# Optimization experiments

Hardware: AMD Instinct MI355X
Metric: run time of the kernel (lower is better)

## Reference

```python
import jax, jax.numpy as jnp
import numpy as np

N_FFT = 256
HOP = 64            # fft_stride
WIN_LEN = 1024      # window_length (samples)
STRIDE = 256        # MPF window stride (samples)
FS = 2000.0
BANDS = [(0.0, 25.0), (25.0, 50.0), (50.0, 100.0), (100.0, 200.0), (200.0, 400.0), (400.0, 1000.0)]


def setup_inputs() -> dict:
    key = jax.random.key(0)
    x = jax.random.normal(key, (8, 32, 16000), dtype=jnp.float32)
    return {"inputs": x}


def _mpf_forward(inputs):
    # --- channelwise STFT (center=False, onesided, hann periodic=False) ---
    window = jnp.asarray(np.hanning(N_FFT), dtype=inputs.dtype)  # matches torch.hann_window(periodic=False)
    wnorm = jnp.linalg.norm(window)
    B, C, T = inputs.shape
    n_frames = 1 + (T - N_FFT) // HOP
    fidx = np.arange(n_frames)[:, None] * HOP + np.arange(N_FFT)[None, :]
    frames = inputs[..., fidx]                       # (B, C, n_frames, n_fft)
    spec = jnp.fft.rfft(frames * window, axis=-1) / wnorm  # (B, C, n_frames, F)
    spec = jnp.swapaxes(spec, -1, -2)                # (B, C, F, n_frames)

    # --- sliding window over STFT frames ---
    size = WIN_LEN // HOP   # 16
    step = STRIDE // HOP    # 4
    n_win = (n_frames - size) // step + 1
    widx = np.arange(n_win)[:, None] * step + np.arange(size)[None, :]
    win = spec[..., widx]                            # (B, C, F, n_win, size)
    x = jnp.transpose(win, (0, 3, 2, 1, 4))          # (B, n_win, F, C, size)

    # --- cross-spectral density: X X^H / size, then |.|^2 ---
    csd = jnp.einsum('btfcw,btfdw->btfcd', x, jnp.conj(x)) / size
    csd = csd.real ** 2 + csd.imag ** 2              # (B, n_win, F, C, C) real

    # --- average FFT bins into frequency bands ---
    freqs = np.fft.rfftfreq(N_FFT, d=1.0 / FS)
    masks_np = np.stack([(freqs > lo) & (freqs <= hi) for lo, hi in BANDS]).astype(np.float32)
    masks = jnp.asarray(masks_np, dtype=csd.dtype)   # (n_bands, F)
    banded = jnp.einsum('btfcd,kf->btkcd', csd, masks) / masks.sum(axis=1)[None, None, :, None, None]

    # --- SPD matrix log via eigh, eigvals floored at 100*eps ---
    eigvals, eigvecs = jnp.linalg.eigh(banded)
    floor = 100.0 * jnp.finfo(banded.dtype).eps
    log_vals = jnp.log(jnp.maximum(eigvals, floor))
    out = jnp.einsum('...ij,...j,...kj->...ik', eigvecs, log_vals, eigvecs)

    # (batch, time, bands, c1, c2) -> (batch, bands, c1, c2, time)
    return jnp.transpose(out, (0, 2, 3, 4, 1))


def reference(inputs) -> jnp.ndarray:
    return _mpf_forward(inputs)
```

## Files before the change

kernel.cpp:

```cpp
#include <hip/hip_runtime.h>
#include <cstddef>

#define NFRM 247
#define NBIN 128
#define NC   32
#define NWIN 58
#define NMAT (8 * NWIN * 6)

__global__ __launch_bounds__(128) void k_stft(const float* __restrict__ x,
                                              float2* __restrict__ spec) {
  const int gid = blockIdx.x;
  const int fr  = gid % NFRM;
  const int bc  = gid / NFRM;
  const int tid = threadIdx.x;

  __shared__ float  xw[256];
  __shared__ float2 tw[256];
  __shared__ float2 Y[256];

  const float* xp = x + ((size_t)bc * 16000 + (size_t)fr * 64);

  #pragma unroll
  for (int k = 0; k < 2; ++k) {
    const int t = tid + k * 128;
    const float wv = 0.5f - 0.5f * __cosf((float)t * 0.024639942f);
    xw[t] = xp[t] * wv * 0.10226200f;
    float sv, cv;
    __sincosf((float)t * 0.024543693f, &sv, &cv);
    tw[t] = make_float2(cv, -sv);
  }
  __syncthreads();

  #pragma unroll
  for (int k = 0; k < 2; ++k) {
    const int e = tid + k * 128;
    const int f0 = e >> 4, t0 = e & 15;
    const int step = (f0 << 4) & 255;
    float re = 0.f, im = 0.f;
    int m = 0;
    #pragma unroll
    for (int t1 = 0; t1 < 16; ++t1) {
      const float v = xw[(t1 << 4) + t0];
      const float2 w = tw[m];
      re = fmaf(v, w.x, re);
      im = fmaf(v, w.y, im);
      m = (m + step) & 255;
    }
    Y[e] = make_float2(re, im);
  }
  __syncthreads();

  const int f = tid + 1;
  const int f0 = f & 15;
  float re = 0.f, im = 0.f;
  int m = 0;
  #pragma unroll
  for (int t0 = 0; t0 < 16; ++t0) {
    const float2 yv = Y[(f0 << 4) + t0];
    const float2 w = tw[m];
    re += yv.x * w.x - yv.y * w.y;
    im += yv.x * w.y + yv.y * w.x;
    m = (m + f) & 255;
  }
  const int b = bc >> 5, c = bc & 31;
  spec[(((size_t)b * NFRM + fr) * NBIN + (f - 1)) * NC + c] = make_float2(re, im);
}

__global__ __launch_bounds__(256) void k_csd(const float2* __restrict__ spec,
                                             float* __restrict__ part, int P) {
  const int bt  = blockIdx.x;
  const int p   = blockIdx.y;
  const int b   = bt / NWIN, t = bt % NWIN;
  const int tid = threadIdx.x;
  const int wv  = tid >> 6;
  const int lane = tid & 63;
  const int i0 = (lane >> 3) * 4;
  const int j0 = (lane & 7) * 4;

  __shared__ __align__(16) char smemraw[32768];
  float2 (*rng)[2][512] = reinterpret_cast<float2 (*)[2][512]>(smemraw);
  float* red = reinterpret_cast<float*>(smemraw);

  float bacc[6][16];
  #pragma unroll
  for (int k = 0; k < 6; ++k)
    #pragma unroll
    for (int e = 0; e < 16; ++e) bacc[k][e] = 0.f;

  const float2* sb = spec + (size_t)b * NFRM * NBIN * NC;
  const int itn = 32 / P;

  #define STG_LOAD(itl, dst)                                                     \
    {                                                                            \
      const int f_ = 1 + wv + 4 * (itn * p + (itl));                             \
      const float2* fp_ = sb + (size_t)(f_ - 1) * NC;                            \
      _Pragma("unroll")                                                          \
      for (int r = 0; r < 8; ++r) {                                              \
        const int e_ = lane + r * 64;                                            \
        dst[r] = fp_[(size_t)(t * 4 + (e_ >> 5)) * (NBIN * NC) + (e_ & 31)];     \
      }                                                                          \
    }

  {
    float2 stg[8];
    STG_LOAD(0, stg)
    float2* Xs = rng[wv][0];
    #pragma unroll
    for (int r = 0; r < 8; ++r) Xs[lane + r * 64] = stg[r];
  }

  for (int itl = 0; itl < itn; ++itl) {
    float2 stg2[8];
    if (itl + 1 < itn) STG_LOAD(itl + 1, stg2)

    const int f = 1 + wv + 4 * (itn * p + itl);
    const float2* Xs = rng[wv][itl & 1];

    float accRe[16], accIm[16];
    #pragma unroll
    for (int e = 0; e < 16; ++e) { accRe[e] = 0.f; accIm[e] = 0.f; }

    #pragma unroll
    for (int s = 0; s < 16; ++s) {
      float2 xi[4], xj[4];
      #pragma unroll
      for (int a = 0; a < 4; ++a) {
        xi[a] = Xs[s * 32 + i0 + a];
        xj[a] = Xs[s * 32 + j0 + a];
      }
      #pragma unroll
      for (int a = 0; a < 4; ++a)
        #pragma unroll
        for (int d = 0; d < 4; ++d) {
          const int e = a * 4 + d;
          accRe[e] = fmaf(xi[a].x, xj[d].x, fmaf(xi[a].y, xj[d].y, accRe[e]));
          accIm[e] = fmaf(xi[a].y, xj[d].x, fmaf(-xi[a].x, xj[d].y, accIm[e]));
        }
    }

    #define ACCB(K) { _Pragma("unroll") \
      for (int e = 0; e < 16; ++e) { float rr = accRe[e], ii = accIm[e]; \
        bacc[K][e] = fmaf(rr, rr, fmaf(ii, ii, bacc[K][e])); } }
    if      (f <= 3)  ACCB(0)
    else if (f <= 6)  ACCB(1)
    else if (f <= 12) ACCB(2)
    else if (f <= 25) ACCB(3)
    else if (f <= 51) ACCB(4)
    else              ACCB(5)
    #undef ACCB

    if (itl + 1 < itn) {
      float2* Xn = rng[wv][(itl + 1) & 1];
      #pragma unroll
      for (int r = 0; r < 8; ++r) Xn[lane + r * 64] = stg2[r];
    }
  }
  #undef STG_LOAD

  __syncthreads();

  for (int w2 = 0; w2 < 4; ++w2) {
    if (wv == w2) {
      #pragma unroll
      for (int k = 0; k < 6; ++k)
        #pragma unroll
        for (int a = 0; a < 4; ++a)
          #pragma unroll
          for (int d = 0; d < 4; ++d) {
            const int idx = k * 1024 + (i0 + a) * 32 + (j0 + d);
            const float v = bacc[k][a * 4 + d];
            if (w2 == 0) red[idx] = v; else red[idx] += v;
          }
    }
    __syncthreads();
  }

  float* op = part + ((size_t)p * (8 * NWIN) + bt) * 6144;
  for (int u = tid; u < 6144; u += 256) {
    const int k = u >> 10;
    float scl;
    if      (k <= 1) scl = 1.f / 768.f;
    else if (k == 2) scl = 1.f / 1536.f;
    else if (k == 3) scl = 1.f / 3328.f;
    else if (k == 4) scl = 1.f / 6656.f;
    else             scl = 1.f / 19712.f;
    op[u] = red[u] * scl;
  }
}

__global__ __launch_bounds__(64) void k_eig(const float* __restrict__ part,
                                            float* __restrict__ eigTmp, int P) {
  const int blk  = blockIdx.x;
  const int lane = threadIdx.x;
  const int h    = lane >> 5;
  const int c    = lane & 31;

  __shared__ float sA[32][36];
  __shared__ float sSc[32];

  for (int u = lane; u < 1024; u += 64) {
    const size_t base = (size_t)blk * 1024 + u;
    float s = 0.f;
    for (int p = 0; p < P; ++p) s += part[(size_t)p * ((size_t)NMAT * 1024) + base];
    sA[u >> 5][u & 31] = s;
  }
  __syncthreads();

  float g[16];
  #pragma unroll
  for (int i = 0; i < 16; ++i) g[i] = sA[16 * h + i][c];

  float n;
  {
    float p0 = 0.f, p1 = 0.f, p2 = 0.f, p3 = 0.f;
    #pragma unroll
    for (int e = 0; e < 16; e += 4) {
      p0 = fmaf(g[e + 0], g[e + 0], p0);
      p1 = fmaf(g[e + 1], g[e + 1], p1);
      p2 = fmaf(g[e + 2], g[e + 2], p2);
      p3 = fmaf(g[e + 3], g[e + 3], p3);
    }
    const float pp = (p0 + p1) + (p2 + p3);
    const float op = __shfl_xor(pp, 32);
    n = h ? (op + pp) : (pp + op);
  }

  const float EPS2 = 1e-7f;
  #pragma unroll 1
  for (int sweep = 0; sweep < 10; ++sweep) {
    int anybad = 0;
    #pragma unroll 1
    for (int m = 1; m < 32; ++m) {
      const int pidx = (lane ^ m) << 2;
      float tmp[16];
      #pragma unroll
      for (int e = 0; e < 16; ++e)
        tmp[e] = __int_as_float(__builtin_amdgcn_ds_bpermute(pidx, __float_as_int(g[e])));
      const float np = __int_as_float(__builtin_amdgcn_ds_bpermute(pidx, __float_as_int(n)));

      float d0 = 0.f, d1 = 0.f, d2 = 0.f, d3 = 0.f;
      #pragma unroll
      for (int e = 0; e < 16; e += 4) {
        d0 = fmaf(g[e + 0], tmp[e + 0], d0);
        d1 = fmaf(g[e + 1], tmp[e + 1], d1);
        d2 = fmaf(g[e + 2], tmp[e + 2], d2);
        d3 = fmaf(g[e + 3], tmp[e + 3], d3);
      }
      const float pp = (d0 + d1) + (d2 + d3);
      const float op = __shfl_xor(pp, 32);
      const float bpq = h ? (op + pp) : (pp + op);

      const int bad = (bpq * bpq > EPS2 * n * np);
      anybad |= bad;
      if (bad) {
        const float tau = (np - n) * 0.5f * __builtin_amdgcn_rcpf(bpq);
        float tf = __builtin_amdgcn_rcpf(fabsf(tau) + __builtin_amdgcn_sqrtf(fmaf(tau, tau, 1.f)));
        if (tau < 0.f) tf = -tf;
        const float cr = __builtin_amdgcn_rsqf(fmaf(tf, tf, 1.f));
        const float sg = -tf * cr;
        n = fmaf(-tf, bpq, n);
        #pragma unroll
        for (int e = 0; e < 16; ++e) g[e] = fmaf(sg, tmp[e], cr * g[e]);
      }
    }
    if (!__any(anybad)) break;
  }

  float nx;
  {
    float p0 = 0.f, p1 = 0.f, p2 = 0.f, p3 = 0.f;
    #pragma unroll
    for (int e = 0; e < 16; e += 4) {
      p0 = fmaf(g[e + 0], g[e + 0], p0);
      p1 = fmaf(g[e + 1], g[e + 1], p1);
      p2 = fmaf(g[e + 2], g[e + 2], p2);
      p3 = fmaf(g[e + 3], g[e + 3], p3);
    }
    const float pp = (p0 + p1) + (p2 + p3);
    const float op = __shfl_xor(pp, 32);
    nx = h ? (op + pp) : (pp + op);
  }
  const float lv = 0.5f * __logf(fmaxf(nx, 1.4210855e-10f));
  const float sc = (nx > 1e-32f) ? (lv * __builtin_amdgcn_rcpf(nx)) : 0.f;

  __syncthreads();
  #pragma unroll
  for (int i = 0; i < 16; ++i) sA[c][16 * h + i] = g[i];
  if (h == 0) sSc[c] = sc;
  __syncthreads();

  float a[32];
  #pragma unroll
  for (int e = 0; e < 32; ++e) a[e] = sSc[e] * sA[e][c];

  float* ob = eigTmp + ((size_t)blk * 1024 + c * 32 + 16 * h);
  #pragma unroll
  for (int q = 0; q < 4; ++q) {
    float4 acc = make_float4(0.f, 0.f, 0.f, 0.f);
    #pragma unroll
    for (int e = 0; e < 32; ++e) {
      const float4 gv = *(const float4*)&sA[e][16 * h + 4 * q];
      acc.x = fmaf(a[e], gv.x, acc.x);
      acc.y = fmaf(a[e], gv.y, acc.y);
      acc.z = fmaf(a[e], gv.z, acc.z);
      acc.w = fmaf(a[e], gv.w, acc.w);
    }
    *(float4*)(ob + 4 * q) = acc;
  }
}

__global__ __launch_bounds__(256) void k_tr(const float* __restrict__ eigTmp,
                                            float* __restrict__ out) {
  const int bk    = blockIdx.x >> 3;
  const int chunk = blockIdx.x & 7;
  const int b = bk / 6, k = bk % 6;
  const int ij0 = chunk * 128;
  const int tid = threadIdx.x;

  __shared__ float tile[128 * 59];

  for (int u = tid; u < 128 * NWIN; u += 256) {
    const int t = u >> 7, ijl = u & 127;
    tile[ijl * 59 + t] = eigTmp[((size_t)(b * NWIN + t) * 6 + k) * 1024 + ij0 + ijl];
  }
  __syncthreads();

  float* ob = out + ((size_t)bk * 1024 + ij0) * NWIN;
  for (int u = tid; u < 128 * NWIN; u += 256) {
    ob[u] = tile[(u / NWIN) * 59 + (u % NWIN)];
  }
}

extern "C" void kernel_launch(void* const* d_in, const int* in_sizes, int n_in,
                              void* d_out, int out_size, void* d_ws, size_t ws_size,
                              hipStream_t stream) {
  const float* x = (const float*)d_in[0];
  float* outp = (float*)d_out;

  const size_t SPEC_B = (size_t)8 * NFRM * NBIN * NC * sizeof(float2);
  const size_t BAND_B = (size_t)NMAT * 1024 * sizeof(float);

  float2* spec   = (float2*)d_ws;
  float*  part   = (float*)((char*)d_ws + SPEC_B);
  float*  eigTmp = (float*)d_ws;

  int P = 1;
  if (ws_size >= SPEC_B + 2 * BAND_B) P = 2;

  k_stft<<<dim3(8 * 32 * NFRM), dim3(128), 0, stream>>>(x, spec);
  k_csd <<<dim3(8 * NWIN, P),   dim3(256), 0, stream>>>(spec, part, P);
  k_eig <<<dim3(NMAT),          dim3(64),  0, stream>>>(part, eigTmp, P);
  k_tr  <<<dim3(48 * 8),        dim3(256), 0, stream>>>(eigTmp, outp);
}
```

Before: 452.7 us.

## Use DPP lane swaps for Jacobi rounds and recurrence twiddles in STFT

In the one-sided Jacobi eigen kernel, the first 15 pairing rounds (xor distances 1..15) now exchange columns with DPP quad-permute and row-mirror ops, replacing ds_bpermute. That removes LDS-path traffic and latency for most rotation rounds, and those rounds are fully unrolled. The STFT kernel also drops its shared twiddle table and computes twiddles with a complex rotation recurrence from one sincos per thread. The recurrence adds small rounding drift over 16 steps and costs some extra registers.

Result: no change. 458.1 us (+1.2%).

```diff
diff --git a/kernel.cpp b/kernel.cpp
--- a/kernel.cpp
+++ b/kernel.cpp
@@ -15,7 +15,6 @@
   const int tid = threadIdx.x;
 
   __shared__ float  xw[256];
-  __shared__ float2 tw[256];
   __shared__ float2 Y[256];
 
   const float* xp = x + ((size_t)bc * 16000 + (size_t)fr * 64);
@@ -25,9 +24,6 @@
     const int t = tid + k * 128;
     const float wv = 0.5f - 0.5f * __cosf((float)t * 0.024639942f);
     xw[t] = xp[t] * wv * 0.10226200f;
-    float sv, cv;
-    __sincosf((float)t * 0.024543693f, &sv, &cv);
-    tw[t] = make_float2(cv, -sv);
   }
   __syncthreads();
 
@@ -35,16 +31,17 @@
   for (int k = 0; k < 2; ++k) {
     const int e = tid + k * 128;
     const int f0 = e >> 4, t0 = e & 15;
-    const int step = (f0 << 4) & 255;
-    float re = 0.f, im = 0.f;
-    int m = 0;
+    float sA, cA;
+    __sincosf((float)f0 * 0.39269908f, &sA, &cA);
+    float wr = 1.f, wi = 0.f, re = 0.f, im = 0.f;
     #pragma unroll
     for (int t1 = 0; t1 < 16; ++t1) {
       const float v = xw[(t1 << 4) + t0];
-      const float2 w = tw[m];
-      re = fmaf(v, w.x, re);
-      im = fmaf(v, w.y, im);
-      m = (m + step) & 255;
+      re = fmaf(v, wr, re);
+      im = fmaf(v, wi, im);
+      const float nwr = fmaf(wi, sA, wr * cA);
+      const float nwi = fmaf(-wr, sA, wi * cA);
+      wr = nwr; wi = nwi;
     }
     Y[e] = make_float2(re, im);
   }
@@ -52,15 +49,17 @@
 
   const int f = tid + 1;
   const int f0 = f & 15;
-  float re = 0.f, im = 0.f;
-  int m = 0;
+  float sB, cB;
+  __sincosf((float)f * 0.024543693f, &sB, &cB);
+  float wr = 1.f, wi = 0.f, re = 0.f, im = 0.f;
   #pragma unroll
   for (int t0 = 0; t0 < 16; ++t0) {
     const float2 yv = Y[(f0 << 4) + t0];
-    const float2 w = tw[m];
-    re += yv.x * w.x - yv.y * w.y;
-    im += yv.x * w.y + yv.y * w.x;
-    m = (m + f) & 255;
+    re += yv.x * wr - yv.y * wi;
+    im += yv.x * wi + yv.y * wr;
+    const float nwr = fmaf(wi, sB, wr * cB);
+    const float nwi = fmaf(-wr, sB, wi * cB);
+    wr = nwr; wi = nwi;
   }
   const int b = bc >> 5, c = bc & 31;
   spec[(((size_t)b * NFRM + fr) * NBIN + (f - 1)) * NC + c] = make_float2(re, im);
@@ -188,6 +187,69 @@
   }
 }
 
+template<int CTRL>
+__device__ __forceinline__ float dppf(float v) {
+  return __int_as_float(__builtin_amdgcn_update_dpp(
+      __float_as_int(v), __float_as_int(v), CTRL, 0xF, 0xF, false));
+}
+
+template<int M>
+__device__ __forceinline__ float lxor(float v) {
+#if __has_builtin(__builtin_amdgcn_update_dpp)
+  constexpr int hi = M & 12, lo = M & 3;
+  constexpr int q  = (hi == 4 || hi == 12) ? (lo ^ 3) : lo;
+  if constexpr (q != 0) {
+    constexpr int QC = (q) | ((1 ^ q) << 2) | ((2 ^ q) << 4) | ((3 ^ q) << 6);
+    v = dppf<QC>(v);
+  }
+  if constexpr (hi == 4)  v = dppf<0x141>(v);
+  if constexpr (hi == 8)  v = dppf<0x128>(v);
+  if constexpr (hi == 12) v = dppf<0x140>(v);
+  return v;
+#else
+  return __shfl_xor(v, M);
+#endif
+}
+
+__device__ __forceinline__ void jpair(float (&g)[16], float& n, int& anybad,
+                                      const int h, const float (&tmp)[16],
+                                      const float np) {
+  float d0 = 0.f, d1 = 0.f, d2 = 0.f, d3 = 0.f;
+  #pragma unroll
+  for (int e = 0; e < 16; e += 4) {
+    d0 = fmaf(g[e + 0], tmp[e + 0], d0);
+    d1 = fmaf(g[e + 1], tmp[e + 1], d1);
+    d2 = fmaf(g[e + 2], tmp[e + 2], d2);
+    d3 = fmaf(g[e + 3], tmp[e + 3], d3);
+  }
+  const float pp = (d0 + d1) + (d2 + d3);
+  const float op = __shfl_xor(pp, 32);
+  const float bpq = h ? (op + pp) : (pp + op);
+
+  const int bad = (bpq * bpq > 1e-7f * n * np);
+  anybad |= bad;
+  if (bad) {
+    const float tau = (np - n) * 0.5f * __builtin_amdgcn_rcpf(bpq);
+    float tf = __builtin_amdgcn_rcpf(fabsf(tau) + __builtin_amdgcn_sqrtf(fmaf(tau, tau, 1.f)));
+    if (tau < 0.f) tf = -tf;
+    const float cr = __builtin_amdgcn_rsqf(fmaf(tf, tf, 1.f));
+    const float sg = -tf * cr;
+    n = fmaf(-tf, bpq, n);
+    #pragma unroll
+    for (int e = 0; e < 16; ++e) g[e] = fmaf(sg, tmp[e], cr * g[e]);
+  }
+}
+
+template<int M>
+__device__ __forceinline__ void round_dpp(float (&g)[16], float& n, int& anybad,
+                                          const int h) {
+  float tmp[16];
+  #pragma unroll
+  for (int e = 0; e < 16; ++e) tmp[e] = lxor<M>(g[e]);
+  const float np = lxor<M>(n);
+  jpair(g, n, anybad, h, tmp, np);
+}
+
 __global__ __launch_bounds__(64) void k_eig(const float* __restrict__ part,
                                             float* __restrict__ eigTmp, int P) {
   const int blk  = blockIdx.x;
@@ -225,43 +287,26 @@
     n = h ? (op + pp) : (pp + op);
   }
 
-  const float EPS2 = 1e-7f;
   #pragma unroll 1
   for (int sweep = 0; sweep < 10; ++sweep) {
     int anybad = 0;
+    round_dpp<1>(g, n, anybad, h);  round_dpp<2>(g, n, anybad, h);
+    round_dpp<3>(g, n, anybad, h);  round_dpp<4>(g, n, anybad, h);
+    round_dpp<5>(g, n, anybad, h);  round_dpp<6>(g, n, anybad, h);
+    round_dpp<7>(g, n, anybad, h);  round_dpp<8>(g, n, anybad, h);
+    round_dpp<9>(g, n, anybad, h);  round_dpp<10>(g, n, anybad, h);
+    round_dpp<11>(g, n, anybad, h); round_dpp<12>(g, n, anybad, h);
+    round_dpp<13>(g, n, anybad, h); round_dpp<14>(g, n, anybad, h);
+    round_dpp<15>(g, n, anybad, h);
     #pragma unroll 1
-    for (int m = 1; m < 32; ++m) {
+    for (int m = 16; m < 32; ++m) {
       const int pidx = (lane ^ m) << 2;
       float tmp[16];
       #pragma unroll
       for (int e = 0; e < 16; ++e)
         tmp[e] = __int_as_float(__builtin_amdgcn_ds_bpermute(pidx, __float_as_int(g[e])));
       const float np = __int_as_float(__builtin_amdgcn_ds_bpermute(pidx, __float_as_int(n)));
-
-      float d0 = 0.f, d1 = 0.f, d2 = 0.f, d3 = 0.f;
-      #pragma unroll
-      for (int e = 0; e < 16; e += 4) {
-        d0 = fmaf(g[e + 0], tmp[e + 0], d0);
-        d1 = fmaf(g[e + 1], tmp[e + 1], d1);
-        d2 = fmaf(g[e + 2], tmp[e + 2], d2);
-        d3 = fmaf(g[e + 3], tmp[e + 3], d3);
-      }
-      const float pp = (d0 + d1) + (d2 + d3);
-      const float op = __shfl_xor(pp, 32);
-      const float bpq = h ? (op + pp) : (pp + op);
-
-      const int bad = (bpq * bpq > EPS2 * n * np);
-      anybad |= bad;
-      if (bad) {
-        const float tau = (np - n) * 0.5f * __builtin_amdgcn_rcpf(bpq);
-        float tf = __builtin_amdgcn_rcpf(fabsf(tau) + __builtin_amdgcn_sqrtf(fmaf(tau, tau, 1.f)));
-        if (tau < 0.f) tf = -tf;
-        const float cr = __builtin_amdgcn_rsqf(fmaf(tf, tf, 1.f));
-        const float sg = -tf * cr;
-        n = fmaf(-tf, bpq, n);
-        #pragma unroll
-        for (int e = 0; e < 16; ++e) g[e] = fmaf(sg, tmp[e], cr * g[e]);
-      }
+      jpair(g, n, anybad, h, tmp, np);
     }
     if (!__any(anybad)) break;
   }
```
